# Performance work log

Hardware: AMD Instinct MI355X
Metric: run time of the kernel (lower is better)

## Reference

```python
import jax, jax.numpy as jnp
import numpy as np

B, LAT, FRAME, HID, E, GH = 4096, 64, 512, 1024, 8, 128
IN1 = LAT + FRAME      # 576, fc1/gate input
IN2 = LAT + HID        # 1088, fc2/fc3 input
OUT = FRAME            # 512, num_future_frames * frame_size


def setup_inputs() -> dict:
    key = jax.random.key(0)
    ks = jax.random.split(key, 16)
    s = lambda fan_in: 1.0 / np.sqrt(fan_in)
    inp = {
        "z": jax.random.normal(ks[0], (B, LAT), jnp.float32),
        "c": jax.random.normal(ks[1], (B, FRAME), jnp.float32),
        # expert-mixed layers: weight [E, in, out], bias [E, out]
        "w0": jax.random.uniform(ks[2], (E, IN1, HID), jnp.float32, -s(IN1), s(IN1)),
        "b0": jax.random.uniform(ks[3], (E, HID), jnp.float32, -s(IN1), s(IN1)),
        "w1": jax.random.uniform(ks[4], (E, IN2, HID), jnp.float32, -s(IN2), s(IN2)),
        "b1": jax.random.uniform(ks[5], (E, HID), jnp.float32, -s(IN2), s(IN2)),
        "w2": jax.random.uniform(ks[6], (E, IN2, OUT), jnp.float32, -s(IN2), s(IN2)),
        "b2": jax.random.uniform(ks[7], (E, OUT), jnp.float32, -s(IN2), s(IN2)),
        # gate MLP
        "gw1": jax.random.uniform(ks[8], (IN1, GH), jnp.float32, -s(IN1), s(IN1)),
        "gb1": jax.random.uniform(ks[9], (GH,), jnp.float32, -s(IN1), s(IN1)),
        "gw2": jax.random.uniform(ks[10], (GH, GH), jnp.float32, -s(GH), s(GH)),
        "gb2": jax.random.uniform(ks[11], (GH,), jnp.float32, -s(GH), s(GH)),
        "gw3": jax.random.uniform(ks[12], (GH, E), jnp.float32, -s(GH), s(GH)),
        "gb3": jax.random.uniform(ks[13], (E,), jnp.float32, -s(GH), s(GH)),
    }
    return inp


def _mixed_layer(coef, x, w, b):
    # per-expert projection then softmax-weighted mix: same math as
    # baddbmm(coef@b, x, (coef@flat(w)).view(B,in,out)) in the original.
    ye = jnp.einsum('bi,eio->beo', x, w)          # [B, E, out]
    return jnp.einsum('be,beo->bo', coef, ye) + coef @ b


def reference(z, c, w0, b0, w1, b1, w2, b2, gw1, gb1, gw2, gb2, gw3, gb3):
    x0 = jnp.concatenate([z, c], axis=1)           # [B, IN1]
    h = jax.nn.elu(x0 @ gw1 + gb1)
    h = jax.nn.elu(h @ gw2 + gb2)
    coef = jax.nn.softmax(h @ gw3 + gb3, axis=1)   # [B, E]

    out = jax.nn.elu(_mixed_layer(coef, x0, w0, b0))
    out = jax.nn.elu(_mixed_layer(coef, jnp.concatenate([z, out], axis=1), w1, b1))
    out = _mixed_layer(coef, jnp.concatenate([z, out], axis=1), w2, b2)
    return out
```

## Files before the change

kernel.cpp:

```cpp
#include <hip/hip_runtime.h>
#include <cstdint>
#include <cstddef>

#define B_    4096
#define LAT   64
#define FRAME 512
#define HID   1024
#define NE    8
#define GH    128
#define IN1   576
#define IN2   1088

typedef _Float16 half8 __attribute__((ext_vector_type(8)));
typedef _Float16 half4 __attribute__((ext_vector_type(4)));
typedef float  f32x4  __attribute__((ext_vector_type(4)));
typedef float  f32x16 __attribute__((ext_vector_type(16)));

__device__ inline void async16(const void* g, void* l) {
  __builtin_amdgcn_global_load_lds(
      (__attribute__((address_space(1))) void*)(void*)g,
      (__attribute__((address_space(3))) void*)l, 16, 0, 0);
}

__device__ inline float elu(float v) { return v > 0.f ? v : expm1f(v); }

__global__ __launch_bounds__(256) void prep_weights(
    const float* __restrict__ w0, const float* __restrict__ w1,
    const float* __restrict__ w2, const float* __restrict__ gw1,
    const float* __restrict__ gw2,
    _Float16* __restrict__ Wt0, _Float16* __restrict__ Wt1,
    _Float16* __restrict__ Wt2, _Float16* __restrict__ gw1T,
    _Float16* __restrict__ gw2T)
{
  __shared__ float t[64][65];
  int bid = blockIdx.x;
  const float* in; _Float16* out; int K, N, kt, nt;
  if (bid < 1152) {
    const int e = bid / 144, rem = bid % 144;
    K = IN1; N = HID; kt = rem / 16; nt = rem % 16;
    in = w0 + (size_t)e * K * N; out = Wt0 + (size_t)e * N * K;
  } else if (bid < 3328) {
    const int i = bid - 1152, e = i / 272, rem = i % 272;
    K = IN2; N = HID; kt = rem / 16; nt = rem % 16;
    in = w1 + (size_t)e * K * N; out = Wt1 + (size_t)e * N * K;
  } else if (bid < 4416) {
    const int i = bid - 3328, e = i / 136, rem = i % 136;
    K = IN2; N = FRAME; kt = rem / 8; nt = rem % 8;
    in = w2 + (size_t)e * K * N; out = Wt2 + (size_t)e * N * K;
  } else if (bid < 4434) {
    const int i = bid - 4416;
    K = IN1; N = GH; kt = i / 2; nt = i % 2;
    in = gw1; out = gw1T;
  } else {
    const int i = bid - 4434;
    K = GH; N = GH; kt = i / 2; nt = i % 2;
    in = gw2; out = gw2T;
  }
  const int k0 = kt * 64, n0 = nt * 64;
  const int tx = threadIdx.x & 63, ty = threadIdx.x >> 6;
  #pragma unroll
  for (int it = 0; it < 16; ++it) {
    const int k = it * 4 + ty;
    t[k][tx] = in[(size_t)(k0 + k) * N + n0 + tx];
  }
  __syncthreads();
  #pragma unroll
  for (int it = 0; it < 16; ++it) {
    const int n = it * 4 + ty;
    out[(size_t)(n0 + n) * K + k0 + tx] = (_Float16)t[tx][n];
  }
}

__global__ __launch_bounds__(256) void gate_mfma(
    const float* __restrict__ z, const float* __restrict__ c,
    const _Float16* __restrict__ gw1T,
    const _Float16* __restrict__ gw2T,
    const float* __restrict__ gb1, const float* __restrict__ gb2,
    const float* __restrict__ gw3, const float* __restrict__ gb3,
    float* __restrict__ coef)
{
  __shared__ _Float16 h_lds[64][136];
  __shared__ float    h2_lds[64][129];
  __shared__ float    gw3s[128 * 8];
  const int tid = threadIdx.x;
  const int wave = tid >> 6, lane = tid & 63;
  const int quad = lane >> 4, l16 = lane & 15;
  const int r0 = blockIdx.x * 64;

  for (int i = tid; i < 128 * 8; i += 256) gw3s[i] = gw3[i];

  f32x4 acc[8];
  #pragma unroll
  for (int nt = 0; nt < 8; ++nt)
    #pragma unroll
    for (int r = 0; r < 4; ++r) acc[nt][r] = 0.f;

  #pragma unroll 2
  for (int s = 0; s < 18; ++s) {
    const int k0 = s * 32;
    half8 af;
    {
      const size_t row = r0 + wave * 16 + l16;
      const float* src = (k0 < LAT) ? z + row * LAT + k0 + quad * 8
                                    : c + row * FRAME + (k0 - LAT) + quad * 8;
      f32x4 lo = *(const f32x4*)src, hi = *(const f32x4*)(src + 4);
      #pragma unroll
      for (int j = 0; j < 4; ++j) { af[j] = (_Float16)lo[j]; af[j + 4] = (_Float16)hi[j]; }
    }
    half8 bfr[8];
    #pragma unroll
    for (int nt = 0; nt < 8; ++nt)
      bfr[nt] = *(const half8*)(gw1T + (size_t)(nt * 16 + l16) * 576 + k0 + quad * 8);
    #pragma unroll
    for (int nt = 0; nt < 8; ++nt)
      acc[nt] = __builtin_amdgcn_mfma_f32_16x16x32_f16(af, bfr[nt], acc[nt], 0, 0, 0);
  }
  #pragma unroll
  for (int nt = 0; nt < 8; ++nt)
    #pragma unroll
    for (int r = 0; r < 4; ++r) {
      const int rowl = wave * 16 + quad * 4 + r;
      const int col = nt * 16 + l16;
      h_lds[rowl][col] = (_Float16)elu(acc[nt][r] + gb1[col]);
    }
  __syncthreads();

  f32x4 acc2[8];
  #pragma unroll
  for (int nt = 0; nt < 8; ++nt)
    #pragma unroll
    for (int r = 0; r < 4; ++r) acc2[nt][r] = 0.f;
  #pragma unroll
  for (int s = 0; s < 4; ++s) {
    const int k0 = s * 32;
    half8 af = *(const half8*)&h_lds[wave * 16 + l16][k0 + quad * 8];
    half8 bfr[8];
    #pragma unroll
    for (int nt = 0; nt < 8; ++nt)
      bfr[nt] = *(const half8*)(gw2T + (size_t)(nt * 16 + l16) * 128 + k0 + quad * 8);
    #pragma unroll
    for (int nt = 0; nt < 8; ++nt)
      acc2[nt] = __builtin_amdgcn_mfma_f32_16x16x32_f16(af, bfr[nt], acc2[nt], 0, 0, 0);
  }
  #pragma unroll
  for (int nt = 0; nt < 8; ++nt)
    #pragma unroll
    for (int r = 0; r < 4; ++r) {
      const int rowl = wave * 16 + quad * 4 + r;
      const int col = nt * 16 + l16;
      h2_lds[rowl][col] = elu(acc2[nt][r] + gb2[col]);
    }
  __syncthreads();

  {
    const int row = tid >> 2, q = tid & 3;
    float l2v[2] = { gb3[2 * q], gb3[2 * q + 1] };
    for (int k = 0; k < 128; ++k) {
      const float hv = h2_lds[row][k];
      l2v[0] += hv * gw3s[k * 8 + 2 * q];
      l2v[1] += hv * gw3s[k * 8 + 2 * q + 1];
    }
    float m = fmaxf(l2v[0], l2v[1]);
    m = fmaxf(m, __shfl_xor(m, 1));
    m = fmaxf(m, __shfl_xor(m, 2));
    float e0 = expf(l2v[0] - m), e1 = expf(l2v[1] - m);
    float s = e0 + e1;
    s += __shfl_xor(s, 1);
    s += __shfl_xor(s, 2);
    const float inv = 1.f / s;
    float2 o = { e0 * inv, e1 * inv };
    *(float2*)&coef[(size_t)(r0 + row) * NE + 2 * q] = o;
  }
}

__global__ __launch_bounds__(256) void build_x1(
    const float* __restrict__ z, const float* __restrict__ c,
    _Float16* __restrict__ x1)
{
  const int idx4 = blockIdx.x * 256 + threadIdx.x;
  const int b = idx4 / (IN1 / 4), j = (idx4 - b * (IN1 / 4)) * 4;
  f32x4 v = (j < LAT) ? *(const f32x4*)(z + (size_t)b * LAT + j)
                      : *(const f32x4*)(c + (size_t)b * FRAME + (j - LAT));
  half4 o;
  #pragma unroll
  for (int q = 0; q < 4; ++q) o[q] = (_Float16)v[q];
  *(half4*)(x1 + (size_t)b * IN1 + j) = o;
}

template<int KDIM, int NOUT, int EG>
__global__ __launch_bounds__(256, 2) void gemm_moe(
    const _Float16* __restrict__ X,
    const _Float16* __restrict__ Wt,
    const float* __restrict__ coef,
    const float* __restrict__ bias,
    float* __restrict__ part)
{
  __shared__ __align__(16) _Float16 As[2][128 * 64];
  __shared__ __align__(16) _Float16 Bs[2][128 * 64];
  __shared__ float coefS[128 * EG];
  __shared__ float biasS[EG * 128];

  const int tid = threadIdx.x;
  const int wave = tid >> 6, lane = tid & 63;
  const int wm = wave & 1, wn = wave >> 1;
  const int l32 = lane & 31, khalf = lane >> 5;
  const int bm0 = blockIdx.x * 128, bn0 = blockIdx.y * 128;
  const int ebase = blockIdx.z * EG;

  for (int i = tid; i < 128 * EG; i += 256)
    coefS[i] = coef[(size_t)(bm0 + i / EG) * NE + ebase + (i % EG)];
  for (int i = tid; i < EG * 128; i += 256)
    biasS[i] = bias[(size_t)(ebase + (i >> 7)) * NOUT + bn0 + (i & 127)];

  const int srow  = wave * 8 + (lane >> 3);
  const int skoff = (((lane & 7) ^ ((lane >> 3) & 7)) * 8);

  #define STAGE_A(k0v, buf) \
    { _Pragma("unroll") \
      for (int it = 0; it < 4; ++it) \
        async16(X + (size_t)(bm0 + it * 32 + srow) * KDIM + (k0v) + skoff, \
                &(buf)[it * 2048 + wave * 512]); }
  #define STAGE_B(ev, k0v, buf) \
    { const size_t eoff = (size_t)(ev) * NOUT * KDIM; \
      _Pragma("unroll") \
      for (int it = 0; it < 4; ++it) \
        async16(Wt + eoff + (size_t)(bn0 + it * 32 + srow) * KDIM + (k0v) + skoff, \
                &(buf)[it * 2048 + wave * 512]); }

  STAGE_A(0, As[0]);
  STAGE_B(ebase, 0, Bs[0]);
  __syncthreads();

  _Float16 ch[2][EG];
  #pragma unroll
  for (int mi = 0; mi < 2; ++mi)
    #pragma unroll
    for (int e = 0; e < EG; ++e)
      ch[mi][e] = (_Float16)coefS[(wm * 64 + mi * 32 + l32) * EG + e];

  f32x16 acc[2][2];
  #pragma unroll
  for (int mi = 0; mi < 2; ++mi)
    #pragma unroll
    for (int ni = 0; ni < 2; ++ni)
      #pragma unroll
      for (int r = 0; r < 16; ++r) acc[mi][ni][r] = 0.f;

  constexpr int K0S = KDIM / 64;
  for (int k0i = 0; k0i < K0S; ++k0i) {
    const int k0 = k0i * 64;
    const int ap = k0i & 1;
    half8 af[4][2];
    #pragma unroll
    for (int ks = 0; ks < 4; ++ks)
      #pragma unroll
      for (int mi = 0; mi < 2; ++mi) {
        const int r = wm * 64 + mi * 32 + l32;
        const int g = (ks * 2 + khalf) ^ (r & 7);
        af[ks][mi] = *(const half8*)&As[ap][r * 64 + g * 8];
      }
    #pragma unroll
    for (int eo = 0; eo < EG; ++eo) {
      if (eo + 1 < EG) {
        STAGE_B(ebase + eo + 1, k0, Bs[(eo + 1) & 1]);
      } else if (k0i + 1 < K0S) {
        STAGE_A(k0 + 64, As[1 - ap]);
        STAGE_B(ebase, k0 + 64, Bs[EG & 1]);
      }
      const _Float16* bsrc = Bs[eo & 1];
      #pragma unroll
      for (int ks = 0; ks < 4; ++ks) {
        half8 bv[2];
        #pragma unroll
        for (int ni = 0; ni < 2; ++ni) {
          const int r = wn * 64 + ni * 32 + l32;
          const int g = (ks * 2 + khalf) ^ (r & 7);
          bv[ni] = *(const half8*)&bsrc[r * 64 + g * 8];
        }
        #pragma unroll
        for (int mi = 0; mi < 2; ++mi) {
          const half8 afs = af[ks][mi] * ch[mi][eo];
          #pragma unroll
          for (int ni = 0; ni < 2; ++ni)
            acc[mi][ni] = __builtin_amdgcn_mfma_f32_32x32x16_f16(
                afs, bv[ni], acc[mi][ni], 0, 0, 0);
        }
      }
      __syncthreads();
    }
  }
  #undef STAGE_A
  #undef STAGE_B

  float* po = part + (size_t)blockIdx.z * B_ * NOUT;
  #pragma unroll
  for (int mi = 0; mi < 2; ++mi)
    #pragma unroll
    for (int ni = 0; ni < 2; ++ni)
      #pragma unroll
      for (int reg = 0; reg < 16; ++reg) {
        const int row_l = (reg & 3) + 8 * (reg >> 2) + 4 * khalf;
        const int m_loc = wm * 64 + mi * 32 + row_l;
        const int n_loc = wn * 64 + ni * 32 + l32;
        float v = acc[mi][ni][reg];
        #pragma unroll
        for (int e = 0; e < EG; ++e)
          v += coefS[m_loc * EG + e] * biasS[e * 128 + n_loc];
        po[(size_t)(bm0 + m_loc) * NOUT + bn0 + n_loc] = v;
      }
}

__global__ __launch_bounds__(256) void expand_x(
    const float* __restrict__ part,
    const float* __restrict__ z,
    _Float16* __restrict__ xn)
{
  const int idx4 = blockIdx.x * 256 + threadIdx.x;
  const int b = idx4 / (IN2 / 4), j = (idx4 - b * (IN2 / 4)) * 4;
  half4 o;
  if (j < LAT) {
    f32x4 v = *(const f32x4*)(z + (size_t)b * LAT + j);
    #pragma unroll
    for (int q = 0; q < 4; ++q) o[q] = (_Float16)v[q];
  } else {
    const int h = j - LAT;
    f32x4 v0 = *(const f32x4*)(part + (size_t)b * HID + h);
    f32x4 v1 = *(const f32x4*)(part + (size_t)B_ * HID + (size_t)b * HID + h);
    #pragma unroll
    for (int q = 0; q < 4; ++q) o[q] = (_Float16)elu(v0[q] + v1[q]);
  }
  *(half4*)(xn + (size_t)b * IN2 + j) = o;
}

__global__ __launch_bounds__(256) void final_out(
    const float* __restrict__ part,
    float* __restrict__ out)
{
  const int idx4 = (blockIdx.x * 256 + threadIdx.x) * 4;
  f32x4 v = *(const f32x4*)(part + idx4);
  #pragma unroll
  for (int s = 1; s < 4; ++s) {
    f32x4 p = *(const f32x4*)(part + (size_t)s * B_ * FRAME + idx4);
    #pragma unroll
    for (int q = 0; q < 4; ++q) v[q] += p[q];
  }
  *(f32x4*)(out + idx4) = v;
}


extern "C" void kernel_launch(void* const* d_in, const int* in_sizes, int n_in,
                              void* d_out, int out_size, void* d_ws, size_t ws_size,
                              hipStream_t stream)
{
  const float* z   = (const float*)d_in[0];
  const float* c   = (const float*)d_in[1];
  const float* w0  = (const float*)d_in[2];
  const float* b0  = (const float*)d_in[3];
  const float* w1  = (const float*)d_in[4];
  const float* b1  = (const float*)d_in[5];
  const float* w2  = (const float*)d_in[6];
  const float* b2  = (const float*)d_in[7];
  const float* gw1 = (const float*)d_in[8];
  const float* gb1 = (const float*)d_in[9];
  const float* gw2 = (const float*)d_in[10];
  const float* gb2 = (const float*)d_in[11];
  const float* gw3 = (const float*)d_in[12];
  const float* gb3 = (const float*)d_in[13];
  float* out = (float*)d_out;
  char* ws = (char*)d_ws;

  float*    coef = (float*)    (ws + 0);
  _Float16* x1   = (_Float16*) (ws + 131072);
  _Float16* x2   = (_Float16*) (ws + 4849664);
  _Float16* x3   = (_Float16*) (ws + 13762560);
  _Float16* Wt0  = (_Float16*) (ws + 22675456);
  _Float16* Wt1  = (_Float16*) (ws + 32112640);
  _Float16* Wt2  = (_Float16*) (ws + 49938432);
  float*    part = (float*)    (ws + 58851328);
  _Float16* gw1T = (_Float16*) (ws + 92405760);
  _Float16* gw2T = (_Float16*) (ws + 92553216);

  prep_weights<<<4438, 256, 0, stream>>>(w0, w1, w2, gw1, gw2,
                                         Wt0, Wt1, Wt2, gw1T, gw2T);
  gate_mfma<<<64, 256, 0, stream>>>(z, c, gw1T, gw2T, gb1, gb2, gw3, gb3, coef);
  build_x1<<<(B_ * IN1 / 4) / 256, 256, 0, stream>>>(z, c, x1);

  gemm_moe<IN1, HID, 4><<<dim3(32, 8, 2), 256, 0, stream>>>(x1, Wt0, coef, b0, part);
  expand_x<<<(B_ * IN2 / 4) / 256, 256, 0, stream>>>(part, z, x2);

  gemm_moe<IN2, HID, 4><<<dim3(32, 8, 2), 256, 0, stream>>>(x2, Wt1, coef, b1, part);
  expand_x<<<(B_ * IN2 / 4) / 256, 256, 0, stream>>>(part, z, x3);

  gemm_moe<IN2, FRAME, 2><<<dim3(32, 4, 4), 256, 0, stream>>>(x3, Wt2, coef, b2, part);
  final_out<<<(B_ * FRAME / 4) / 256, 256, 0, stream>>>(part, out);
}
```

Before: 356.6 us.

## Switch MoE GEMM to 16x16x32 MFMA, single-buffer A, vectorize weight transpose

Replaces the 32x32x16 MFMA tiling in the expert-mixed GEMM with 16x16x32 MFMAs over a 4x4 fragment grid per wave, changing the accumulator layout and epilogue indexing. The A tile moves from a double buffer to a single buffer loaded at the top of each K step, followed by a barrier. This drops the cross-K prefetch of A and of the first expert's B tile, so load latency is exposed at every K step. The weight prep transpose also switches to 16-byte vector loads and half4 stores.

```diff
diff --git a/kernel.cpp b/kernel.cpp
--- a/kernel.cpp
+++ b/kernel.cpp
@@ -14,7 +14,6 @@
 typedef _Float16 half8 __attribute__((ext_vector_type(8)));
 typedef _Float16 half4 __attribute__((ext_vector_type(4)));
 typedef float  f32x4  __attribute__((ext_vector_type(4)));
-typedef float  f32x16 __attribute__((ext_vector_type(16)));
 
 __device__ inline void async16(const void* g, void* l) {
   __builtin_amdgcn_global_load_lds(
@@ -57,17 +56,22 @@
     in = gw2; out = gw2T;
   }
   const int k0 = kt * 64, n0 = nt * 64;
-  const int tx = threadIdx.x & 63, ty = threadIdx.x >> 6;
-  #pragma unroll
-  for (int it = 0; it < 16; ++it) {
-    const int k = it * 4 + ty;
-    t[k][tx] = in[(size_t)(k0 + k) * N + n0 + tx];
+  const int lr = threadIdx.x >> 4;
+  const int lc = (threadIdx.x & 15) * 4;
+  #pragma unroll
+  for (int rr = 0; rr < 4; ++rr) {
+    const int k = rr * 16 + lr;
+    f32x4 v = *(const f32x4*)(in + (size_t)(k0 + k) * N + n0 + lc);
+    t[k][lc] = v[0]; t[k][lc + 1] = v[1]; t[k][lc + 2] = v[2]; t[k][lc + 3] = v[3];
   }
   __syncthreads();
   #pragma unroll
-  for (int it = 0; it < 16; ++it) {
-    const int n = it * 4 + ty;
-    out[(size_t)(n0 + n) * K + k0 + tx] = (_Float16)t[tx][n];
+  for (int rr = 0; rr < 4; ++rr) {
+    const int n = rr * 16 + lr;
+    half4 o;
+    #pragma unroll
+    for (int q = 0; q < 4; ++q) o[q] = (_Float16)t[lc + q][n];
+    *(half4*)(out + (size_t)(n0 + n) * K + k0 + lc) = o;
   }
 }
 
@@ -195,7 +199,7 @@
     const float* __restrict__ bias,
     float* __restrict__ part)
 {
-  __shared__ __align__(16) _Float16 As[2][128 * 64];
+  __shared__ __align__(16) _Float16 As[128 * 64];
   __shared__ __align__(16) _Float16 Bs[2][128 * 64];
   __shared__ float coefS[128 * EG];
   __shared__ float biasS[EG * 128];
@@ -203,7 +207,7 @@
   const int tid = threadIdx.x;
   const int wave = tid >> 6, lane = tid & 63;
   const int wm = wave & 1, wn = wave >> 1;
-  const int l32 = lane & 31, khalf = lane >> 5;
+  const int quad = lane >> 4, l16 = lane & 15;
   const int bm0 = blockIdx.x * 128, bn0 = blockIdx.y * 128;
   const int ebase = blockIdx.z * EG;
 
@@ -211,103 +215,100 @@
     coefS[i] = coef[(size_t)(bm0 + i / EG) * NE + ebase + (i % EG)];
   for (int i = tid; i < EG * 128; i += 256)
     biasS[i] = bias[(size_t)(ebase + (i >> 7)) * NOUT + bn0 + (i & 127)];
+  __syncthreads();
+
+  _Float16 ch[4][EG];
+  #pragma unroll
+  for (int mi = 0; mi < 4; ++mi)
+    #pragma unroll
+    for (int e = 0; e < EG; ++e)
+      ch[mi][e] = (_Float16)coefS[(wm * 64 + mi * 16 + l16) * EG + e];
+
+  f32x4 acc[4][4];
+  #pragma unroll
+  for (int mi = 0; mi < 4; ++mi)
+    #pragma unroll
+    for (int ni = 0; ni < 4; ++ni)
+      #pragma unroll
+      for (int r = 0; r < 4; ++r) acc[mi][ni][r] = 0.f;
 
   const int srow  = wave * 8 + (lane >> 3);
   const int skoff = (((lane & 7) ^ ((lane >> 3) & 7)) * 8);
-
-  #define STAGE_A(k0v, buf) \
-    { _Pragma("unroll") \
-      for (int it = 0; it < 4; ++it) \
-        async16(X + (size_t)(bm0 + it * 32 + srow) * KDIM + (k0v) + skoff, \
-                &(buf)[it * 2048 + wave * 512]); }
-  #define STAGE_B(ev, k0v, buf) \
-    { const size_t eoff = (size_t)(ev) * NOUT * KDIM; \
-      _Pragma("unroll") \
-      for (int it = 0; it < 4; ++it) \
-        async16(Wt + eoff + (size_t)(bn0 + it * 32 + srow) * KDIM + (k0v) + skoff, \
-                &(buf)[it * 2048 + wave * 512]); }
-
-  STAGE_A(0, As[0]);
-  STAGE_B(ebase, 0, Bs[0]);
-  __syncthreads();
-
-  _Float16 ch[2][EG];
-  #pragma unroll
-  for (int mi = 0; mi < 2; ++mi)
-    #pragma unroll
-    for (int e = 0; e < EG; ++e)
-      ch[mi][e] = (_Float16)coefS[(wm * 64 + mi * 32 + l32) * EG + e];
-
-  f32x16 acc[2][2];
-  #pragma unroll
-  for (int mi = 0; mi < 2; ++mi)
-    #pragma unroll
-    for (int ni = 0; ni < 2; ++ni)
-      #pragma unroll
-      for (int r = 0; r < 16; ++r) acc[mi][ni][r] = 0.f;
 
   constexpr int K0S = KDIM / 64;
   for (int k0i = 0; k0i < K0S; ++k0i) {
     const int k0 = k0i * 64;
-    const int ap = k0i & 1;
-    half8 af[4][2];
-    #pragma unroll
-    for (int ks = 0; ks < 4; ++ks)
-      #pragma unroll
-      for (int mi = 0; mi < 2; ++mi) {
-        const int r = wm * 64 + mi * 32 + l32;
-        const int g = (ks * 2 + khalf) ^ (r & 7);
-        af[ks][mi] = *(const half8*)&As[ap][r * 64 + g * 8];
+    #pragma unroll
+    for (int it = 0; it < 4; ++it)
+      async16(X + (size_t)(bm0 + it * 32 + srow) * KDIM + k0 + skoff,
+              &As[it * 2048 + wave * 512]);
+    {
+      const size_t eoff = (size_t)ebase * NOUT * KDIM;
+      #pragma unroll
+      for (int it = 0; it < 4; ++it)
+        async16(Wt + eoff + (size_t)(bn0 + it * 32 + srow) * KDIM + k0 + skoff,
+                &Bs[0][it * 2048 + wave * 512]);
+    }
+    __syncthreads();
+
+    half8 af[2][4];
+    #pragma unroll
+    for (int ks = 0; ks < 2; ++ks)
+      #pragma unroll
+      for (int mi = 0; mi < 4; ++mi) {
+        const int r = wm * 64 + mi * 16 + l16;
+        const int g = (ks * 4 + quad) ^ (r & 7);
+        af[ks][mi] = *(const half8*)&As[r * 64 + g * 8];
       }
+
     #pragma unroll
     for (int eo = 0; eo < EG; ++eo) {
       if (eo + 1 < EG) {
-        STAGE_B(ebase + eo + 1, k0, Bs[(eo + 1) & 1]);
-      } else if (k0i + 1 < K0S) {
-        STAGE_A(k0 + 64, As[1 - ap]);
-        STAGE_B(ebase, k0 + 64, Bs[EG & 1]);
+        const size_t eoff = (size_t)(ebase + eo + 1) * NOUT * KDIM;
+        #pragma unroll
+        for (int it = 0; it < 4; ++it)
+          async16(Wt + eoff + (size_t)(bn0 + it * 32 + srow) * KDIM + k0 + skoff,
+                  &Bs[(eo + 1) & 1][it * 2048 + wave * 512]);
       }
       const _Float16* bsrc = Bs[eo & 1];
       #pragma unroll
-      for (int ks = 0; ks < 4; ++ks) {
-        half8 bv[2];
+      for (int ks = 0; ks < 2; ++ks) {
+        half8 bv[4];
         #pragma unroll
-        for (int ni = 0; ni < 2; ++ni) {
-          const int r = wn * 64 + ni * 32 + l32;
-          const int g = (ks * 2 + khalf) ^ (r & 7);
+        for (int ni = 0; ni < 4; ++ni) {
+          const int r = wn * 64 + ni * 16 + l16;
+          const int g = (ks * 4 + quad) ^ (r & 7);
           bv[ni] = *(const half8*)&bsrc[r * 64 + g * 8];
         }
         #pragma unroll
-        for (int mi = 0; mi < 2; ++mi) {
+        for (int mi = 0; mi < 4; ++mi) {
           const half8 afs = af[ks][mi] * ch[mi][eo];
           #pragma unroll
-          for (int ni = 0; ni < 2; ++ni)
-            acc[mi][ni] = __builtin_amdgcn_mfma_f32_32x32x16_f16(
+          for (int ni = 0; ni < 4; ++ni)
+            acc[mi][ni] = __builtin_amdgcn_mfma_f32_16x16x32_f16(
                 afs, bv[ni], acc[mi][ni], 0, 0, 0);
         }
       }
       __syncthreads();
     }
   }
-  #undef STAGE_A
-  #undef STAGE_B
 
   float* po = part + (size_t)blockIdx.z * B_ * NOUT;
   #pragma unroll
-  for (int mi = 0; mi < 2; ++mi)
-    #pragma unroll
-    for (int ni = 0; ni < 2; ++ni)
-      #pragma unroll
-      for (int reg = 0; reg < 16; ++reg) {
-        const int row_l = (reg & 3) + 8 * (reg >> 2) + 4 * khalf;
-        const int m_loc = wm * 64 + mi * 32 + row_l;
-        const int n_loc = wn * 64 + ni * 32 + l32;
-        float v = acc[mi][ni][reg];
+  for (int mi = 0; mi < 4; ++mi)
+    #pragma unroll
+    for (int r = 0; r < 4; ++r) {
+      const int m_loc = wm * 64 + mi * 16 + quad * 4 + r;
+      #pragma unroll
+      for (int ni = 0; ni < 4; ++ni) {
+        const int n_loc = wn * 64 + ni * 16 + l16;
+        float v = acc[mi][ni][r];
         #pragma unroll
         for (int e = 0; e < EG; ++e)
           v += coefS[m_loc * EG + e] * biasS[e * 128 + n_loc];
         po[(size_t)(bm0 + m_loc) * NOUT + bn0 + n_loc] = v;
       }
+    }
 }
 
 __global__ __launch_bounds__(256) void expand_x(
```

Result: faster. 341.9 us (-4.1%).
